# Kernel tuning notes

Hardware: AMD Instinct MI355X
Metric: run time of the kernel (lower is better)

Reference implementation:

```python
import jax, jax.numpy as jnp
import numpy as np

DIM = 1024
NUM_HEADS = 16
HEAD_DIM = DIM // NUM_HEADS           # 64
WIDTH_SCALE = 0.5                      # set via configure_width in the source
CUR_HD = int(HEAD_DIM * WIDTH_SCALE)   # 32
CUR_DIM = CUR_HD * NUM_HEADS           # 512
SCALE = (HEAD_DIM ** -0.5) / (WIDTH_SCALE ** 0.5)
B, N = 2, 2048


def setup_inputs() -> dict:
    key = jax.random.key(0)
    k1, k2, k3 = jax.random.split(key, 3)
    x = jax.random.normal(k1, (B, N, DIM), dtype=jnp.float32)
    # 0.02 init keeps pre-softmax logits in a realistic range
    w_qkv = jax.random.normal(k2, (3 * DIM, DIM), dtype=jnp.float32) * 0.02
    w_proj = jax.random.normal(k3, (DIM, DIM), dtype=jnp.float32) * 0.02
    b_proj = jnp.zeros((DIM,), dtype=jnp.float32)
    return {"x": x, "w_qkv": w_qkv, "w_proj": w_proj, "b_proj": b_proj}


def reference(x, w_qkv, w_proj, b_proj):
    Bb, Nn, C = x.shape
    cq = 3 * CUR_DIM
    # dynamic-width slice of the fused QKV weight (qkv_bias=False)
    qkv = x @ w_qkv[:cq, :].T                              # (B, N, 3*CUR_DIM)
    qkv = qkv.reshape(Bb, Nn, 3, NUM_HEADS, CUR_HD).transpose(2, 0, 3, 1, 4)
    q, k, v = qkv[0], qkv[1], qkv[2]                       # (B, H, N, hd)
    attn = jax.nn.softmax(jnp.einsum('bhnd,bhmd->bhnm', q, k) * SCALE, axis=-1)
    o = jnp.einsum('bhnm,bhmd->bhnd', attn, v)             # (B, H, N, hd)
    o = o.transpose(0, 2, 1, 3).reshape(Bb, Nn, CUR_DIM)
    # proj uses only its first CUR_DIM input columns
    return o @ w_proj[:, :CUR_DIM].T + b_proj
```

## Files before the change

kernel.cpp:

```cpp
#include <hip/hip_runtime.h>

typedef __bf16 bf16;
typedef __bf16 bf16x8 __attribute__((ext_vector_type(8)));
typedef __bf16 bf16x4 __attribute__((ext_vector_type(4)));
typedef __bf16 bf16x2 __attribute__((ext_vector_type(2)));
typedef float  f32x4  __attribute__((ext_vector_type(4)));
typedef float  f32x16 __attribute__((ext_vector_type(16)));
typedef unsigned int uint32;

constexpr int DIM_  = 1024;
constexpr int NH    = 16;
constexpr int CHD   = 32;
constexpr int CDIM  = 512;
constexpr int CQ    = 1536;
constexpr int NSEQ  = 2048;
constexpr int M_    = 4096;
constexpr float ATT_SCALE = 0.17677669529663687f;
constexpr float QS_LOG2 = ATT_SCALE * 1.4426950408889634f;

__device__ inline void gload16(const bf16* g, bf16* l) {
    __builtin_amdgcn_global_load_lds((const __attribute__((address_space(1))) void*)g,
                                     (__attribute__((address_space(3))) void*)l, 16, 0, 0);
}

constexpr int NX4 = M_ * DIM_ / 4;
constexpr int NW4 = CQ * DIM_ / 4;
constexpr int NP4 = DIM_ * (CDIM / 4);
__global__ void cast_fused(const float* __restrict__ x, const float* __restrict__ wq,
                           const float* __restrict__ wp, bf16* __restrict__ xb,
                           bf16* __restrict__ wqb, bf16* __restrict__ wpb) {
    int i = blockIdx.x * blockDim.x + threadIdx.x;
    const float4* src;
    bf16x4* dst;
    if (i < NX4) {
        src = reinterpret_cast<const float4*>(x) + i;
        dst = reinterpret_cast<bf16x4*>(xb) + i;
    } else if (i < NX4 + NW4) {
        int j = i - NX4;
        src = reinterpret_cast<const float4*>(wq) + j;
        dst = reinterpret_cast<bf16x4*>(wqb) + j;
    } else {
        int j = i - (NX4 + NW4);
        int c = j >> 7, j4 = j & 127;
        src = reinterpret_cast<const float4*>(wp + c * DIM_) + j4;
        dst = reinterpret_cast<bf16x4*>(wpb + c * CDIM) + j4;
    }
    float4 v = *src;
    bf16x4 o = { (bf16)v.x, (bf16)v.y, (bf16)v.z, (bf16)v.w };
    *dst = o;
}

template<int KDIM, int MODE>
__launch_bounds__(256)
__global__ void gemm_nt(const bf16* __restrict__ A, const bf16* __restrict__ Bm,
                        bf16* __restrict__ qbo, bf16* __restrict__ kbo, bf16* __restrict__ vto,
                        float* __restrict__ Cf, const float* __restrict__ bias) {
    __shared__ __align__(16) bf16 SMEM[24576];
    bf16* As = SMEM;
    bf16* Bs = SMEM + 16384;
    const int tid = threadIdx.x;
    const int w = tid >> 6, lane = tid & 63;
    const int m0 = blockIdx.x * 128, n0 = blockIdx.y * 64;
    const int wr = (w >> 1) * 64, wc = (w & 1) * 32;
    const int cl = lane & 15, hi = lane >> 4;
    const int swz = cl & 7;

    const int srow = lane >> 3, schk = (lane & 7) ^ (lane >> 3);
    const bf16* gaA = A  + (m0 + srow) * KDIM + schk * 8;
    const bf16* gbB = Bm + (n0 + srow) * KDIM + schk * 8;

    constexpr int KT = KDIM / 64;

    auto stage = [&](int kt, int b) {
#pragma unroll
        for (int i = 0; i < 4; ++i)
            gload16(gaA + (w * 4 + i) * 8 * KDIM + kt * 64, As + b * 8192 + (w * 4 + i) * 512);
#pragma unroll
        for (int i = 0; i < 2; ++i)
            gload16(gbB + (w * 2 + i) * 8 * KDIM + kt * 64, Bs + b * 4096 + (w * 2 + i) * 512);
    };
    stage(0, 0);
    __syncthreads();

    f32x4 acc[4][2] = {};

    for (int kt = 0; kt < KT; ++kt) {
        if (kt + 1 < KT) stage(kt + 1, (kt + 1) & 1);
        const bf16* as = As + (kt & 1) * 8192;
        const bf16* bs = Bs + (kt & 1) * 4096;
#pragma unroll
        for (int kh = 0; kh < 2; ++kh) {
            const int ck = ((kh * 4 + hi) ^ swz) * 8;
            bf16x8 af[4], bfr[2];
#pragma unroll
            for (int i = 0; i < 4; ++i)
                af[i]  = *reinterpret_cast<const bf16x8*>(as + (wr + i * 16 + cl) * 64 + ck);
#pragma unroll
            for (int j = 0; j < 2; ++j)
                bfr[j] = *reinterpret_cast<const bf16x8*>(bs + (wc + j * 16 + cl) * 64 + ck);
#pragma unroll
            for (int i = 0; i < 4; ++i)
#pragma unroll
                for (int j = 0; j < 2; ++j)
                    acc[i][j] = __builtin_amdgcn_mfma_f32_16x16x32_bf16(af[i], bfr[j], acc[i][j], 0, 0, 0);
        }
        __syncthreads();
    }

    const int rg = hi * 4;
    if constexpr (MODE == 2) {
#pragma unroll
        for (int i = 0; i < 4; ++i)
#pragma unroll
            for (int j = 0; j < 2; ++j) {
                const int row = m0 + wr + i * 16 + rg;
                const int col = n0 + wc + j * 16 + cl;
                const float bv = bias[col];
#pragma unroll
                for (int r = 0; r < 4; ++r)
                    Cf[(row + r) * DIM_ + col] = acc[i][j][r] + bv;
            }
    } else {
        const int sec = n0 >> 9;
        if (sec == 2) {
#pragma unroll
            for (int i = 0; i < 4; ++i)
#pragma unroll
                for (int j = 0; j < 2; ++j) {
                    const int row = m0 + wr + i * 16 + rg;
                    const int col = n0 + wc + j * 16 + cl;
                    const int rem = col & 511;
                    const int h = rem >> 5, d = rem & 31;
                    const int bb = row >> 11, pos = row & 2047;
                    const int bh = bb * NH + h;
                    bf16x4 st;
#pragma unroll
                    for (int r = 0; r < 4; ++r) st[r] = (bf16)acc[i][j][r];
                    *reinterpret_cast<bf16x4*>(vto + (bh * CHD + d) * NSEQ + pos) = st;
                }
        } else {
            const float sc = sec ? 1.0f : QS_LOG2;
            __syncthreads();
#pragma unroll
            for (int i = 0; i < 4; ++i)
#pragma unroll
                for (int j = 0; j < 2; ++j)
#pragma unroll
                    for (int r = 0; r < 4; ++r)
                        SMEM[(wr + i * 16 + rg + r) * 72 + wc + j * 16 + cl] =
                            (bf16)(acc[i][j][r] * sc);
            __syncthreads();
            const int row = tid >> 1, ch = (tid & 1) * 32;
            const int m = m0 + row, bb = m >> 11, pos = m & 2047;
            const int col0 = n0 + ch;
            const int h = (col0 & 511) >> 5;
            bf16* dst = (sec ? kbo : qbo) + ((bb * NH + h) * NSEQ + pos) * CHD;
#pragma unroll
            for (int v4 = 0; v4 < 4; ++v4)
                *reinterpret_cast<bf16x8*>(dst + v4 * 8) =
                    *reinterpret_cast<const bf16x8*>(SMEM + row * 72 + ch + v4 * 8);
        }
    }
}

__device__ inline uint32 pkbf(float lo, float hi) {
    bf16x2 t = { (bf16)lo, (bf16)hi };
    return __builtin_bit_cast(uint32, t);
}

__launch_bounds__(512, 4)
__global__ void flash_kernel(const bf16* __restrict__ qb, const bf16* __restrict__ kb,
                             const bf16* __restrict__ vt, bf16* __restrict__ outb) {
    __shared__ __align__(16) char smem[65536];
    const int tid = threadIdx.x;
    const int w = tid >> 6, lane = tid & 63;
    const int lq = lane & 31, hi = lane >> 5;
    const int p = w & 3, half = w >> 2;

    const int blin = blockIdx.x;
    const int xcd = blin & 7, within = blin >> 3;
    const int head = xcd * 4 + (within >> 4);
    const int qblk = within & 15;
    const int q0 = qblk * 128 + p * 32;

    const bf16* Q = qb + head * (NSEQ * CHD);
    const bf16* K = kb + head * (NSEQ * CHD);
    const bf16* V = vt + head * (CHD * NSEQ);

    const bf16x8 qf0 = *reinterpret_cast<const bf16x8*>(Q + (q0 + lq) * CHD + hi * 8);
    const bf16x8 qf1 = *reinterpret_cast<const bf16x8*>(Q + (q0 + lq) * CHD + 16 + hi * 8);

    char* base = smem + half * 32768;
    const bf16* srcK = K + (half * 1024 + p * 32 + lq) * CHD + hi * 8;
    const bf16* srcV = V + lq * NSEQ + half * 1024 + p * 32 + hi * 8;

    auto stage = [&](int t) {
        char* b = base + (t & 1) * 16384;
        gload16(srcK + t * 128 * CHD,      (bf16*)(b + (2 * p) * 1024));
        gload16(srcK + t * 128 * CHD + 16, (bf16*)(b + (2 * p + 1) * 1024));
        gload16(srcV + t * 128,            (bf16*)(b + 8192 + (2 * p) * 1024));
        gload16(srcV + t * 128 + 16,       (bf16*)(b + 8192 + (2 * p + 1) * 1024));
    };
    stage(0);
    __syncthreads();

    f32x16 o = {};
    float rs[4] = {};
    const f32x16 zero16 = {};

    for (int t = 0; t < 8; ++t) {
        if (t < 7) stage(t + 1);
        char* buf = base + (t & 1) * 16384;
#pragma unroll
        for (int h = 0; h < 4; ++h) {
            const bf16x8 k0 = *reinterpret_cast<const bf16x8*>(buf + (2 * h) * 1024 + lane * 16);
            const bf16x8 k1 = *reinterpret_cast<const bf16x8*>(buf + (2 * h + 1) * 1024 + lane * 16);
            __builtin_amdgcn_s_setprio(1);
            f32x16 s = __builtin_amdgcn_mfma_f32_32x32x16_bf16(k0, qf0, zero16, 0, 0, 0);
            s = __builtin_amdgcn_mfma_f32_32x32x16_bf16(k1, qf1, s, 0, 0, 0);
            __builtin_amdgcn_s_setprio(0);

#pragma unroll
            for (int cc = 0; cc < 2; ++cc) {
                const int b8 = cc * 8;
                float e[8];
#pragma unroll
                for (int j = 0; j < 8; ++j) e[j] = __builtin_amdgcn_exp2f(s[b8 + j]);
#pragma unroll
                for (int j = 0; j < 8; ++j) rs[j & 3] += e[j];
                uint32 u0 = pkbf(e[0], e[1]);
                uint32 u1 = pkbf(e[2], e[3]);
                uint32 u2 = pkbf(e[4], e[5]);
                uint32 u3 = pkbf(e[6], e[7]);
                asm volatile("v_permlane32_swap_b32 %0, %1" : "+v"(u0), "+v"(u2));
                asm volatile("v_permlane32_swap_b32 %0, %1" : "+v"(u1), "+v"(u3));
                union { uint32 u[4]; bf16x8 v; } pb;
                pb.u[0] = u0; pb.u[1] = u1; pb.u[2] = u2; pb.u[3] = u3;
                const bf16x8 vf = *reinterpret_cast<const bf16x8*>(buf + 8192 + (2 * h + cc) * 1024 + lane * 16);
                __builtin_amdgcn_s_setprio(1);
                o = __builtin_amdgcn_mfma_f32_32x32x16_bf16(vf, pb.v, o, 0, 0, 0);
                __builtin_amdgcn_s_setprio(0);
            }
        }
        __syncthreads();
    }

    float ls = (rs[0] + rs[1]) + (rs[2] + rs[3]);
    ls += __shfl_xor(ls, 32);

    float* Mo = (float*)(smem + p * 4608);
    float* Ml = (float*)(smem + p * 4608 + 4096);
    if (half) {
#pragma unroll
        for (int r = 0; r < 16; ++r) Mo[r * 64 + lane] = o[r];
        Ml[lane] = ls;
    }
    __syncthreads();
    if (!half) {
        const float inv = 1.f / (ls + Ml[lane]);
        const int bb = head >> 4, hh = head & 15;
        const int row = bb * NSEQ + q0 + lq;
        const int colb = hh * CHD;
#pragma unroll
        for (int rq = 0; rq < 4; ++rq) {
            bf16x4 st;
#pragma unroll
            for (int ri = 0; ri < 4; ++ri)
                st[ri] = (bf16)((o[rq * 4 + ri] + Mo[(rq * 4 + ri) * 64 + lane]) * inv);
            *reinterpret_cast<bf16x4*>(outb + row * CDIM + colb + rq * 8 + hi * 4) = st;
        }
    }
}

extern "C" void kernel_launch(void* const* d_in, const int* in_sizes, int n_in,
                              void* d_out, int out_size, void* d_ws, size_t ws_size,
                              hipStream_t stream) {
    const float* x      = (const float*)d_in[0];
    const float* w_qkv  = (const float*)d_in[1];
    const float* w_proj = (const float*)d_in[2];
    const float* b_proj = (const float*)d_in[3];
    float* out = (float*)d_out;

    char* ws = (char*)d_ws;
    bf16* xb  = (bf16*)(ws);
    bf16* wqb = (bf16*)(ws + 8388608);
    bf16* wpb = (bf16*)(ws + 11534336);
    bf16* qb  = (bf16*)(ws + 25165824);
    bf16* kb  = (bf16*)(ws + 29360128);
    bf16* vt  = (bf16*)(ws + 33554432);
    bf16* ob  = (bf16*)(ws + 37748736);

    cast_fused<<<(NX4 + NW4 + NP4) / 256, 256, 0, stream>>>(x, w_qkv, w_proj, xb, wqb, wpb);

    gemm_nt<DIM_, 1><<<dim3(32, 24), 256, 0, stream>>>(xb, wqb, qb, kb, vt, nullptr, nullptr);

    flash_kernel<<<512, 512, 0, stream>>>(qb, kb, vt, ob);

    gemm_nt<CDIM, 2><<<dim3(32, 16), 256, 0, stream>>>(ob, wpb, nullptr, nullptr, nullptr, out, b_proj);
}
```

Before: 68.70 us.

## Split flash attention into 2-wave blocks with per-wave private KV pipelines

Restructures the attention kernel from 512-thread blocks (4 query strips × 2 KV halves sharing staged tiles) to 128-thread blocks, one query strip per block with two waves each covering half the keys. Each wave streams its own KV tiles through a private double buffer and waits with s_waitcnt vmcnt, so the per-tile __syncthreads disappear. The cost is that K/V tiles are no longer shared across four query strips, which quadruples L2/global KV traffic per query and adds more, smaller steps (32 iterations of 32 keys).

Measured after the change: 90.19 us. 1.31x slower.

```diff
diff --git a/kernel.cpp b/kernel.cpp
--- a/kernel.cpp
+++ b/kernel.cpp
@@ -168,20 +168,19 @@
     return __builtin_bit_cast(uint32, t);
 }
 
-__launch_bounds__(512, 4)
+__launch_bounds__(128, 4)
 __global__ void flash_kernel(const bf16* __restrict__ qb, const bf16* __restrict__ kb,
                              const bf16* __restrict__ vt, bf16* __restrict__ outb) {
-    __shared__ __align__(16) char smem[65536];
+    __shared__ __align__(16) char smem[16384];
     const int tid = threadIdx.x;
     const int w = tid >> 6, lane = tid & 63;
     const int lq = lane & 31, hi = lane >> 5;
-    const int p = w & 3, half = w >> 2;
 
     const int blin = blockIdx.x;
     const int xcd = blin & 7, within = blin >> 3;
-    const int head = xcd * 4 + (within >> 4);
-    const int qblk = within & 15;
-    const int q0 = qblk * 128 + p * 32;
+    const int head = xcd * 4 + (within >> 6);
+    const int strip = within & 63;
+    const int q0 = strip * 32;
 
     const bf16* Q = qb + head * (NSEQ * CHD);
     const bf16* K = kb + head * (NSEQ * CHD);
@@ -190,73 +189,79 @@
     const bf16x8 qf0 = *reinterpret_cast<const bf16x8*>(Q + (q0 + lq) * CHD + hi * 8);
     const bf16x8 qf1 = *reinterpret_cast<const bf16x8*>(Q + (q0 + lq) * CHD + 16 + hi * 8);
 
-    char* base = smem + half * 32768;
-    const bf16* srcK = K + (half * 1024 + p * 32 + lq) * CHD + hi * 8;
-    const bf16* srcV = V + lq * NSEQ + half * 1024 + p * 32 + hi * 8;
+    char* base = smem + w * 8192;
+    const int kvbeg = w * 1024;
+    const bf16* srcK = K + (kvbeg + lq) * CHD + hi * 8;
+    const bf16* srcV = V + lq * NSEQ + kvbeg + hi * 8;
 
     auto stage = [&](int t) {
-        char* b = base + (t & 1) * 16384;
-        gload16(srcK + t * 128 * CHD,      (bf16*)(b + (2 * p) * 1024));
-        gload16(srcK + t * 128 * CHD + 16, (bf16*)(b + (2 * p + 1) * 1024));
-        gload16(srcV + t * 128,            (bf16*)(b + 8192 + (2 * p) * 1024));
-        gload16(srcV + t * 128 + 16,       (bf16*)(b + 8192 + (2 * p + 1) * 1024));
+        char* b = base + (t & 1) * 4096;
+        gload16(srcK + t * 32 * CHD,      (bf16*)(b));
+        gload16(srcK + t * 32 * CHD + 16, (bf16*)(b + 1024));
+        gload16(srcV + t * 32,            (bf16*)(b + 2048));
+        gload16(srcV + t * 32 + 16,       (bf16*)(b + 3072));
     };
     stage(0);
-    __syncthreads();
 
     f32x16 o = {};
     float rs[4] = {};
     const f32x16 zero16 = {};
 
-    for (int t = 0; t < 8; ++t) {
-        if (t < 7) stage(t + 1);
-        char* buf = base + (t & 1) * 16384;
-#pragma unroll
-        for (int h = 0; h < 4; ++h) {
-            const bf16x8 k0 = *reinterpret_cast<const bf16x8*>(buf + (2 * h) * 1024 + lane * 16);
-            const bf16x8 k1 = *reinterpret_cast<const bf16x8*>(buf + (2 * h + 1) * 1024 + lane * 16);
+    for (int t = 0; t < 32; ++t) {
+        if (t < 31) {
+            stage(t + 1);
+            asm volatile("s_waitcnt vmcnt(4)" ::: "memory");
+        } else {
+            asm volatile("s_waitcnt vmcnt(0)" ::: "memory");
+        }
+        __builtin_amdgcn_sched_barrier(0);
+
+        char* b = base + (t & 1) * 4096;
+        const bf16x8 k0 = *reinterpret_cast<const bf16x8*>(b + lane * 16);
+        const bf16x8 k1 = *reinterpret_cast<const bf16x8*>(b + 1024 + lane * 16);
+        __builtin_amdgcn_s_setprio(1);
+        f32x16 s = __builtin_amdgcn_mfma_f32_32x32x16_bf16(k0, qf0, zero16, 0, 0, 0);
+        s = __builtin_amdgcn_mfma_f32_32x32x16_bf16(k1, qf1, s, 0, 0, 0);
+        __builtin_amdgcn_s_setprio(0);
+
+#pragma unroll
+        for (int cc = 0; cc < 2; ++cc) {
+            const int b8 = cc * 8;
+            float e[8];
+#pragma unroll
+            for (int j = 0; j < 8; ++j) e[j] = __builtin_amdgcn_exp2f(s[b8 + j]);
+#pragma unroll
+            for (int j = 0; j < 8; ++j) rs[j & 3] += e[j];
+            uint32 u0 = pkbf(e[0], e[1]);
+            uint32 u1 = pkbf(e[2], e[3]);
+            uint32 u2 = pkbf(e[4], e[5]);
+            uint32 u3 = pkbf(e[6], e[7]);
+            asm volatile("v_permlane32_swap_b32 %0, %1" : "+v"(u0), "+v"(u2));
+            asm volatile("v_permlane32_swap_b32 %0, %1" : "+v"(u1), "+v"(u3));
+            union { uint32 u[4]; bf16x8 v; } pb;
+            pb.u[0] = u0; pb.u[1] = u1; pb.u[2] = u2; pb.u[3] = u3;
+            const bf16x8 vf = *reinterpret_cast<const bf16x8*>(b + 2048 + cc * 1024 + lane * 16);
             __builtin_amdgcn_s_setprio(1);
-            f32x16 s = __builtin_amdgcn_mfma_f32_32x32x16_bf16(k0, qf0, zero16, 0, 0, 0);
-            s = __builtin_amdgcn_mfma_f32_32x32x16_bf16(k1, qf1, s, 0, 0, 0);
+            o = __builtin_amdgcn_mfma_f32_32x32x16_bf16(vf, pb.v, o, 0, 0, 0);
             __builtin_amdgcn_s_setprio(0);
-
-#pragma unroll
-            for (int cc = 0; cc < 2; ++cc) {
-                const int b8 = cc * 8;
-                float e[8];
-#pragma unroll
-                for (int j = 0; j < 8; ++j) e[j] = __builtin_amdgcn_exp2f(s[b8 + j]);
-#pragma unroll
-                for (int j = 0; j < 8; ++j) rs[j & 3] += e[j];
-                uint32 u0 = pkbf(e[0], e[1]);
-                uint32 u1 = pkbf(e[2], e[3]);
-                uint32 u2 = pkbf(e[4], e[5]);
-                uint32 u3 = pkbf(e[6], e[7]);
-                asm volatile("v_permlane32_swap_b32 %0, %1" : "+v"(u0), "+v"(u2));
-                asm volatile("v_permlane32_swap_b32 %0, %1" : "+v"(u1), "+v"(u3));
-                union { uint32 u[4]; bf16x8 v; } pb;
-                pb.u[0] = u0; pb.u[1] = u1; pb.u[2] = u2; pb.u[3] = u3;
-                const bf16x8 vf = *reinterpret_cast<const bf16x8*>(buf + 8192 + (2 * h + cc) * 1024 + lane * 16);
-                __builtin_amdgcn_s_setprio(1);
-                o = __builtin_amdgcn_mfma_f32_32x32x16_bf16(vf, pb.v, o, 0, 0, 0);
-                __builtin_amdgcn_s_setprio(0);
-            }
-        }
-        __syncthreads();
+        }
     }
 
     float ls = (rs[0] + rs[1]) + (rs[2] + rs[3]);
     ls += __shfl_xor(ls, 32);
 
-    float* Mo = (float*)(smem + p * 4608);
-    float* Ml = (float*)(smem + p * 4608 + 4096);
-    if (half) {
+    __syncthreads();
+    if (w) {
+        float* Mo = (float*)(smem);
+        float* Ml = (float*)(smem + 4096);
 #pragma unroll
         for (int r = 0; r < 16; ++r) Mo[r * 64 + lane] = o[r];
         Ml[lane] = ls;
     }
     __syncthreads();
-    if (!half) {
+    if (!w) {
+        const float* Mo = (const float*)(smem);
+        const float* Ml = (const float*)(smem + 4096);
         const float inv = 1.f / (ls + Ml[lane]);
         const int bb = head >> 4, hh = head & 15;
         const int row = bb * NSEQ + q0 + lq;
@@ -294,7 +299,7 @@
 
     gemm_nt<DIM_, 1><<<dim3(32, 24), 256, 0, stream>>>(xb, wqb, qb, kb, vt, nullptr, nullptr);
 
-    flash_kernel<<<512, 512, 0, stream>>>(qb, kb, vt, ob);
+    flash_kernel<<<2048, 128, 0, stream>>>(qb, kb, vt, ob);
 
     gemm_nt<CDIM, 2><<<dim3(32, 16), 256, 0, stream>>>(ob, wpb, nullptr, nullptr, nullptr, out, b_proj);
 }
```
